# Kernel tuning notes

Hardware: AMD Instinct MI355X
Metric: run time of the kernel (lower is better)

Reference implementation:

```python
import jax, jax.numpy as jnp
import numpy as np

BN_EPS = 1e-5


def _conv1d(x, w, b):
    # x: (B, C, T), w: (O, C, K), torch Conv1d with padding=K//2
    k = w.shape[-1]
    p = k // 2
    out = jax.lax.conv_general_dilated(
        x, w, window_strides=(1,), padding=[(p, p)],
        dimension_numbers=("NCH", "OIH", "NCH"))
    return out + b[None, :, None]


def setup_inputs() -> dict:
    key = jax.random.key(0)
    ks = jax.random.split(key, 16)
    B, C, T, H, NC = 32, 13, 2048, 128, 10
    d = {
        "x": jax.random.normal(ks[0], (B, C, T), jnp.float32),
        "w1": jax.random.normal(ks[1], (H, C, 10), jnp.float32) * 0.1,
        "b1": jax.random.normal(ks[2], (H,), jnp.float32) * 0.1,
        "w2": jax.random.normal(ks[3], (H, C, 20), jnp.float32) * 0.1,
        "b2": jax.random.normal(ks[4], (H,), jnp.float32) * 0.1,
        "w3": jax.random.normal(ks[5], (H, C, 30), jnp.float32) * 0.1,
        "b3": jax.random.normal(ks[6], (H,), jnp.float32) * 0.1,
        "w4": jax.random.normal(ks[7], (H, C, 40), jnp.float32) * 0.1,
        "b4": jax.random.normal(ks[8], (H,), jnp.float32) * 0.1,
        "bn_gamma": jax.random.uniform(ks[9], (4 * H,), jnp.float32, 0.5, 1.5),
        "bn_beta": jax.random.normal(ks[10], (4 * H,), jnp.float32) * 0.1,
        "bn_mean": jnp.zeros((4 * H,), jnp.float32),
        "bn_var": jnp.ones((4 * H,), jnp.float32),
        "logreg_w": jax.random.normal(ks[11], (NC, 4 * H), jnp.float32) * 0.05,
        "logreg_b": jax.random.normal(ks[12], (NC,), jnp.float32) * 0.1,
        "dec_w": jax.random.normal(ks[13], (1, 4 * H), jnp.float32) * 0.05,
        "dec_b": jax.random.normal(ks[14], (1,), jnp.float32) * 0.1,
    }
    return d


def reference(x, w1, b1, w2, b2, w3, b3, w4, b4,
              bn_gamma, bn_beta, bn_mean, bn_var,
              logreg_w, logreg_b, dec_w, dec_b):
    # --- multi-scale shapelet conv + per-prefix cumulative max pooling ---
    feats = []
    for w, b in ((w1, b1), (w2, b2), (w3, b3), (w4, b4)):
        f = _conv1d(x, w, b)                      # (B, H, T+1) (even kernels)
        # original loop: for t in 1..T_out-1 take max over f[:, :, :t]
        # == running (cumulative) max, dropping the last prefix
        cm = jax.lax.cummax(f, axis=2)[:, :, :-1]  # (B, H, T)
        feats.append(jnp.transpose(cm, (0, 2, 1)))  # (B, T, H)
    features = jnp.concatenate(feats, axis=-1)      # (B, T, 4H)

    # --- BatchNorm1d over feature channels (eval mode), dropout = identity ---
    inv = jax.lax.rsqrt(bn_var + BN_EPS)
    features = (features - bn_mean) * (inv * bn_gamma) + bn_beta

    # --- classification head and halting head ---
    logits = jnp.einsum("btf,cf->btc", features, logreg_w) + logreg_b  # (B,T,NC)
    deltas = jnp.einsum("btf,of->bto", features, dec_w) + dec_b        # (B,T,1)
    deltas = jax.nn.softmax(deltas[..., 0], axis=1)                    # (B,T)

    # --- attention budget: pt_t = delta_t * budget_{t-1}; budget decays ---
    B = deltas.shape[0]
    q = 1.0 - deltas                                # (B, T)
    cp = jnp.cumprod(q[:, 1:], axis=1)              # prod_{s=1..t} q_s
    budget = jnp.concatenate([jnp.ones((B, 1), deltas.dtype), cp], axis=1)
    pts_loop = deltas[:, 1:] * budget[:, :-1]       # (B, T-1)
    pts = jnp.concatenate([pts_loop, budget[:, -1:]], axis=1)  # (B, T)

    probs = jax.nn.softmax(logits, axis=-1)  # temperature = 1
    return probs, pts
```

## Files before the change

kernel.cpp:

```cpp
#include <hip/hip_runtime.h>
#include <math.h>

#define NEG_INF (-3.402823466e38f)

typedef float f32x4 __attribute__((ext_vector_type(4)));
typedef short bf16x8 __attribute__((ext_vector_type(8)));

__device__ __forceinline__ unsigned short f2bf(float f) {
    unsigned int u = __float_as_uint(f);
    unsigned int r = (u + 0x7FFFu + ((u >> 16) & 1u)) >> 16;
    return (unsigned short)r;
}
__device__ __forceinline__ float bf2f(unsigned short s) {
    return __uint_as_float(((unsigned int)s) << 16);
}
__device__ __forceinline__ unsigned int pack2(float a, float b) {
    return (unsigned int)f2bf(a) | ((unsigned int)f2bf(b) << 16);
}
__device__ __forceinline__ int swz(int a) { return a ^ (((a >> 5) & 7) << 4); }

__global__ __launch_bounds__(512) void prep_kernel(
    const float* __restrict__ x,
    const float* __restrict__ w1, const float* __restrict__ w2,
    const float* __restrict__ w3, const float* __restrict__ w4,
    const float* __restrict__ bn_gamma, const float* __restrict__ bn_beta,
    const float* __restrict__ bn_mean, const float* __restrict__ bn_var,
    const float* __restrict__ lw, const float* __restrict__ lb,
    const float* __restrict__ dw, const float* __restrict__ db,
    unsigned short* __restrict__ xT, unsigned short* __restrict__ Bfrag,
    unsigned short* __restrict__ hfrag, float* __restrict__ bfo,
    float* __restrict__ dbfo)
{
    int bid = blockIdx.x;
    int tid = threadIdx.x;
    if (bid < 136) {
        int idx = bid * 512 + tid;
        int b = idx / 2176, r = idx - b * 2176;
        int t = r - 20;
        unsigned short row[16];
#pragma unroll
        for (int c = 0; c < 16; ++c) {
            float v = (c < 13 && t >= 0 && t < 2048) ? x[((size_t)(b * 13 + c)) * 2048 + t] : 0.f;
            row[c] = f2bf(v);
        }
        uint4* dst = (uint4*)(xT + (size_t)idx * 16);
        uint4 v0, v1;
        v0.x = row[0] | ((unsigned)row[1] << 16);  v0.y = row[2] | ((unsigned)row[3] << 16);
        v0.z = row[4] | ((unsigned)row[5] << 16);  v0.w = row[6] | ((unsigned)row[7] << 16);
        v1.x = row[8] | ((unsigned)row[9] << 16);  v1.y = row[10] | ((unsigned)row[11] << 16);
        v1.z = row[12] | ((unsigned)row[13] << 16); v1.w = row[14] | ((unsigned)row[15] << 16);
        dst[0] = v0; dst[1] = v1;
    } else if (bid < 186) {
        int idx = (bid - 136) * 512 + tid;
        int lane = idx & 63, frag = idx >> 6;
        int rel, Kc; const float* w;
        if (frag < 40)       { rel = frag;       w = w1; Kc = 10; }
        else if (frag < 120) { rel = frag - 40;  w = w2; Kc = 20; }
        else if (frag < 240) { rel = frag - 120; w = w3; Kc = 30; }
        else                 { rel = frag - 240; w = w4; Kc = 40; }
        int kh = Kc / 2;
        int ht = rel / kh;
        int k0 = rel - ht * kh;
        int h = ht * 16 + (lane & 15);
        int dk = lane >> 5;
        int cbase = 8 * ((lane >> 4) & 1);
        int k = 2 * k0 + dk;
        unsigned short e[8];
#pragma unroll
        for (int j = 0; j < 8; ++j) {
            int c = cbase + j;
            float v = (c < 13) ? w[((size_t)h * 13 + c) * Kc + k] : 0.f;
            e[j] = f2bf(v);
        }
        uint4 pk;
        pk.x = e[0] | ((unsigned)e[1] << 16); pk.y = e[2] | ((unsigned)e[3] << 16);
        pk.z = e[4] | ((unsigned)e[5] << 16); pk.w = e[6] | ((unsigned)e[7] << 16);
        *(uint4*)(Bfrag + (size_t)frag * 512 + lane * 8) = pk;
    } else if (bid == 186) {
        __shared__ float sh[512];
        int j = tid;
        float s = rsqrtf(bn_var[j] + 1e-5f) * bn_gamma[j];
        float shift = bn_beta[j] - bn_mean[j] * s;
        sh[j] = shift;
        __syncthreads();
        if (j < 10) {
            float acc = lb[j];
            for (int q = 0; q < 512; ++q) acc += sh[q] * lw[j * 512 + q];
            bfo[j] = acc;
        } else if (j == 10) {
            float acc = db[0];
            for (int q = 0; q < 512; ++q) acc += sh[q] * dw[q];
            dbfo[0] = acc;
        }
    } else {
        int idx = (bid - 187) * 512 + tid;
        int lane = idx & 63, frag = idx >> 6;
        int n = lane & 15;
        unsigned short e[8];
#pragma unroll
        for (int jj = 0; jj < 8; ++jj) {
            int k = frag * 32 + 8 * (lane >> 4) + jj;
            float s = rsqrtf(bn_var[k] + 1e-5f) * bn_gamma[k];
            float v = (n < 10) ? lw[n * 512 + k] * s : (n == 10) ? dw[k] * s : 0.f;
            e[jj] = f2bf(v);
        }
        uint4 pk;
        pk.x = e[0] | ((unsigned)e[1] << 16); pk.y = e[2] | ((unsigned)e[3] << 16);
        pk.z = e[4] | ((unsigned)e[5] << 16); pk.w = e[6] | ((unsigned)e[7] << 16);
        *(uint4*)(hfrag + (size_t)frag * 512 + lane * 8) = pk;
    }
}

__global__ __launch_bounds__(256, 4) void conv_mfma(
    const unsigned short* __restrict__ xT, const unsigned short* __restrict__ Bfrag,
    const float* __restrict__ b1, const float* __restrict__ b2,
    const float* __restrict__ b3, const float* __restrict__ b4,
    unsigned short* __restrict__ feat, unsigned short* __restrict__ totals)
{
    __shared__ __align__(16) unsigned short lds[2688 + 2 * 64 * 132];
    unsigned short* xs = lds;
    unsigned int* stg32 = (unsigned int*)(lds + 2688);
    const int tid = threadIdx.x;
    const int tq = blockIdx.x & 15;
    const int scale = (blockIdx.x >> 4) & 3;
    const int b = blockIdx.x >> 6;
    const int kh_tab[4] = {5, 10, 15, 20};
    const int so_tab[4] = {0, 40, 120, 240};
    const int KH = kh_tab[scale];
    const int P = 5 * (scale + 1);
    const float* bias = (scale == 0) ? b1 : (scale == 1) ? b2 : (scale == 2) ? b3 : b4;

    const unsigned short* src = xT + ((size_t)b * 2176 + tq * 128) * 16;
#pragma unroll
    for (int it = 0; it < 2; ++it) {
        int c = it * 256 + tid;
        if (c < 336) {
            uint4 v = *(const uint4*)(src + c * 8);
            *(uint4*)((char*)xs + swz(c * 16)) = v;
        }
    }
    __syncthreads();

    const int lane = tid & 63;
    const int wave = tid >> 6;
    const int hgrp = wave & 1;
    const int twq = wave >> 1;
    const int l15 = lane & 15;
    const int g4 = lane >> 4;

    const unsigned short* bfr = Bfrag + ((size_t)(so_tab[scale] + hgrp * 4 * KH)) * 512 + lane * 8;
    float bv[4];
#pragma unroll
    for (int ht = 0; ht < 4; ++ht) bv[ht] = bias[hgrp * 64 + ht * 16 + l15];

    int abase = ((20 - P) + twq * 64 + l15 + (lane >> 5)) * 32 + (g4 & 1) * 16;

    f32x4 acc[4][4];
#pragma unroll
    for (int ht = 0; ht < 4; ++ht)
#pragma unroll
        for (int tt = 0; tt < 4; ++tt)
            acc[ht][tt] = (f32x4){bv[ht], bv[ht], bv[ht], bv[ht]};

#pragma unroll 1
    for (int k0 = 0; k0 < KH; ++k0) {
        bf16x8 B[4], A[4];
#pragma unroll
        for (int ht = 0; ht < 4; ++ht)
            B[ht] = *(const bf16x8*)(bfr + (size_t)(ht * KH + k0) * 512);
#pragma unroll
        for (int tt = 0; tt < 4; ++tt)
            A[tt] = *(const bf16x8*)((const char*)xs + swz(abase + tt * 512 + k0 * 64));
#pragma unroll
        for (int ht = 0; ht < 4; ++ht)
#pragma unroll
            for (int tt = 0; tt < 4; ++tt)
                acc[ht][tt] = __builtin_amdgcn_mfma_f32_16x16x32_bf16(A[tt], B[ht], acc[ht][tt], 0, 0, 0);
    }

    float carry[4] = {NEG_INF, NEG_INF, NEG_INF, NEG_INF};
    const int rq = tq * 2 + twq;
    const int col = hgrp * 64 + l15;

#pragma unroll
    for (int tt = 0; tt < 4; ++tt) {
#pragma unroll
        for (int ht = 0; ht < 4; ++ht) {
            f32x4 v = acc[ht][tt];
            float s0 = v.x;
            float s1 = fmaxf(v.y, s0);
            float s2 = fmaxf(v.z, s1);
            float s3 = fmaxf(v.w, s2);
            float inc = s3;
            float o = __shfl_up(inc, 16); if (lane >= 16) inc = fmaxf(inc, o);
            o = __shfl_up(inc, 32);       if (lane >= 32) inc = fmaxf(inc, o);
            float pre = __shfl_up(inc, 16);
            float base = (lane >= 16) ? fmaxf(carry[ht], pre) : carry[ht];
            s0 = fmaxf(s0, base); s1 = fmaxf(s1, base);
            s2 = fmaxf(s2, base); s3 = fmaxf(s3, base);
            float tot = __shfl(inc, l15 + 48);
            carry[ht] = fmaxf(carry[ht], tot);
            int r2 = twq * 32 + tt * 8 + 2 * g4;
            int cc = col + ht * 16;
            stg32[r2 * 132 + cc]       = pack2(s0, s1);
            stg32[(r2 + 1) * 132 + cc] = pack2(s2, s3);
        }
    }
    if (lane < 16) {
#pragma unroll
        for (int ht = 0; ht < 4; ++ht) {
            int j = scale * 128 + hgrp * 64 + ht * 16 + l15;
            totals[((size_t)b * 32 + rq) * 512 + j] = f2bf(carry[ht]);
        }
    }
    __syncthreads();

    size_t grow = (size_t)b * 2048 + tq * 128;
#pragma unroll
    for (int i = 0; i < 4; ++i) {
        int e = i * 256 + tid;
        int r2 = e >> 4, q = e & 15;
        const unsigned int* p = stg32 + r2 * 132 + q * 8;
        uint4 da = *(const uint4*)(p);
        uint4 db = *(const uint4*)(p + 4);
        uint4 ev, od;
        ev.x = (da.x & 0xffffu) | (da.y << 16);
        ev.y = (da.z & 0xffffu) | (da.w << 16);
        ev.z = (db.x & 0xffffu) | (db.y << 16);
        ev.w = (db.z & 0xffffu) | (db.w << 16);
        od.x = (da.x >> 16) | (da.y & 0xffff0000u);
        od.y = (da.z >> 16) | (da.w & 0xffff0000u);
        od.z = (db.x >> 16) | (db.y & 0xffff0000u);
        od.w = (db.z >> 16) | (db.w & 0xffff0000u);
        size_t base = (grow + 2 * r2) * 512 + scale * 128 + q * 8;
        *(uint4*)(feat + base)       = ev;
        *(uint4*)(feat + base + 512) = od;
    }
}

__global__ __launch_bounds__(256) void head_kernel(
    const unsigned short* __restrict__ feat, const unsigned short* __restrict__ totals,
    const unsigned short* __restrict__ hfrag, const float* __restrict__ bfo,
    const float* __restrict__ dbfo, float* __restrict__ probs,
    float* __restrict__ delta_raw)
{
    __shared__ float pfs[512];
    int b = blockIdx.x >> 5;
    int tc = blockIdx.x & 31;
    int tid = threadIdx.x;
    int lane = tid & 63;
    int wave = tid >> 6;

    for (int j = tid; j < 512; j += 256) {
        float run = NEG_INF;
        for (int qq = 0; qq < tc; ++qq)
            run = fmaxf(run, bf2f(totals[((size_t)b * 32 + qq) * 512 + j]));
        pfs[j] = run;
    }
    __syncthreads();

    bf16x8 Bf[16];
#pragma unroll
    for (int k0 = 0; k0 < 16; ++k0)
        Bf[k0] = *(const bf16x8*)(hfrag + (size_t)k0 * 512 + lane * 8);

    const int n = lane & 15;
    const int g4 = lane >> 4;
    const int tb = tc * 64 + wave * 16;
    const unsigned short* fb = feat + ((size_t)b * 2048 + tb + n) * 512 + 8 * g4;

    float biasv = (n < 10) ? bfo[n] : (n == 10) ? dbfo[0] : 0.f;
    f32x4 acc = (f32x4){biasv, biasv, biasv, biasv};

#pragma unroll
    for (int k0 = 0; k0 < 16; ++k0) {
        bf16x8 a = *(const bf16x8*)(fb + k0 * 32);
        const float* pp = pfs + k0 * 32 + 8 * g4;
        union { unsigned int u[4]; bf16x8 v; } aw;
#pragma unroll
        for (int i = 0; i < 4; ++i) {
            float lo = fmaxf(bf2f((unsigned short)a[2 * i]),     pp[2 * i]);
            float hi = fmaxf(bf2f((unsigned short)a[2 * i + 1]), pp[2 * i + 1]);
            aw.u[i] = (__float_as_uint(lo) >> 16) | (__float_as_uint(hi) & 0xFFFF0000u);
        }
        acc = __builtin_amdgcn_mfma_f32_16x16x32_bf16(aw.v, Bf[k0], acc, 0, 0, 0);
    }

#pragma unroll
    for (int r = 0; r < 4; ++r) {
        float v = acc[r];
        float vm = (n < 10) ? v : NEG_INF;
#pragma unroll
        for (int off = 1; off < 16; off <<= 1)
            vm = fmaxf(vm, __shfl_xor(vm, off, 16));
        float e = (n < 10) ? __expf(v - vm) : 0.f;
        float s = e;
#pragma unroll
        for (int off = 1; off < 16; off <<= 1)
            s += __shfl_xor(s, off, 16);
        int t = tb + g4 * 4 + r;
        if (n < 10) probs[((size_t)b * 2048 + t) * 10 + n] = e / s;
        if (n == 10) delta_raw[b * 2048 + t] = v;
    }
}

__global__ __launch_bounds__(256) void budget_kernel(
    const float* __restrict__ delta_raw, float* __restrict__ pts)
{
    __shared__ float ds[2048];
    __shared__ float red[8];
    int b = blockIdx.x;
    int tid = threadIdx.x;
    int lane = tid & 63, wid = tid >> 6;
    const float* row = delta_raw + b * 2048;
    int base = tid * 8;
    float d[8];
#pragma unroll
    for (int i = 0; i < 8; ++i) d[i] = row[base + i];
    float m = d[0];
#pragma unroll
    for (int i = 1; i < 8; ++i) m = fmaxf(m, d[i]);
#pragma unroll
    for (int off = 1; off < 64; off <<= 1) m = fmaxf(m, __shfl_xor(m, off));
    if (lane == 0) red[wid] = m;
    __syncthreads();
    m = fmaxf(fmaxf(red[0], red[1]), fmaxf(red[2], red[3]));
    float s = 0.f;
#pragma unroll
    for (int i = 0; i < 8; ++i) { d[i] = __expf(d[i] - m); s += d[i]; }
#pragma unroll
    for (int off = 1; off < 64; off <<= 1) s += __shfl_xor(s, off);
    if (lane == 0) red[4 + wid] = s;
    __syncthreads();
    float inv = 1.f / (red[4] + red[5] + red[6] + red[7]);
    float g[8], p = 1.f;
#pragma unroll
    for (int i = 0; i < 8; ++i) {
        d[i] *= inv;
        ds[base + i] = d[i];
        float gv = (base + i == 0) ? 1.f : (1.f - d[i]);
        p *= gv;
        g[i] = p;
    }
    float sp = p;
#pragma unroll
    for (int off = 1; off < 64; off <<= 1) {
        float o = __shfl_up(sp, off);
        if (lane >= off) sp *= o;
    }
    float pre_t = __shfl_up(sp, 1);
    if (lane == 0) pre_t = 1.f;
    if (lane == 63) red[wid] = sp;
    __syncthreads();
    float wpre = 1.f;
#pragma unroll
    for (int w = 0; w < 4; ++w) if (w < wid) wpre *= red[w];
    float pre = wpre * pre_t;
#pragma unroll
    for (int i = 0; i < 8; ++i) {
        int t = base + i;
        float budget = pre * g[i];
        float pt = (t < 2047) ? ds[t + 1] * budget : budget;
        pts[b * 2048 + t] = pt;
    }
}

extern "C" void kernel_launch(void* const* d_in, const int* in_sizes, int n_in,
                              void* d_out, int out_size, void* d_ws, size_t ws_size,
                              hipStream_t stream)
{
    const float* x     = (const float*)d_in[0];
    const float* w1    = (const float*)d_in[1];
    const float* b1    = (const float*)d_in[2];
    const float* w2    = (const float*)d_in[3];
    const float* b2    = (const float*)d_in[4];
    const float* w3    = (const float*)d_in[5];
    const float* b3    = (const float*)d_in[6];
    const float* w4    = (const float*)d_in[7];
    const float* b4    = (const float*)d_in[8];
    const float* gamma = (const float*)d_in[9];
    const float* beta  = (const float*)d_in[10];
    const float* mean  = (const float*)d_in[11];
    const float* var   = (const float*)d_in[12];
    const float* lw    = (const float*)d_in[13];
    const float* lb    = (const float*)d_in[14];
    const float* dw    = (const float*)d_in[15];
    const float* db    = (const float*)d_in[16];

    char* ws = (char*)d_ws;
    unsigned short* feat   = (unsigned short*)ws;
    unsigned short* xT     = (unsigned short*)(ws + 67108864);
    unsigned short* Bfrag  = (unsigned short*)(ws + 69337088);
    unsigned short* totals = (unsigned short*)(ws + 69746688);
    float* draw   = (float*)(ws + 70795264);
    unsigned short* hfrag = (unsigned short*)(ws + 71057408);
    float* bfo    = (float*)(ws + 71073792);
    float* dbfo   = (float*)(ws + 71073856);

    float* probs = (float*)d_out;
    float* pts   = probs + (size_t)32 * 2048 * 10;

    hipLaunchKernelGGL(prep_kernel, dim3(189), dim3(512), 0, stream,
                       x, w1, w2, w3, w4, gamma, beta, mean, var,
                       lw, lb, dw, db, xT, Bfrag, hfrag, bfo, dbfo);
    hipLaunchKernelGGL(conv_mfma, dim3(2048), dim3(256), 0, stream,
                       xT, Bfrag, b1, b2, b3, b4, feat, totals);
    hipLaunchKernelGGL(head_kernel, dim3(1024), dim3(256), 0, stream,
                       feat, totals, hfrag, bfo, dbfo, probs, draw);
    hipLaunchKernelGGL(budget_kernel, dim3(32), dim3(256), 0, stream, draw, pts);
}
```

Baseline: 87.42 us.

## Double-buffer MFMA operand loads and halve conv epilogue staging LDS

The conv kernel's K loop now software-pipelines the global B-fragment and LDS A-fragment loads, fetching the next step's operands while the current MFMAs run. The epilogue keeps the cummax results in the accumulator registers and stages them through a half-size LDS buffer in two passes, one per time-wave group, with nontemporal global stores. The occupancy hint in launch bounds drops from 4 to 2 waves per SIMD to allow more registers for the doubled operand buffers. In exchange it adds an extra barrier and a serialized two-pass epilogue, and occupancy may fall.

```diff
diff --git a/kernel.cpp b/kernel.cpp
--- a/kernel.cpp
+++ b/kernel.cpp
@@ -5,6 +5,7 @@
 
 typedef float f32x4 __attribute__((ext_vector_type(4)));
 typedef short bf16x8 __attribute__((ext_vector_type(8)));
+typedef unsigned int u32x4 __attribute__((ext_vector_type(4)));
 
 __device__ __forceinline__ unsigned short f2bf(float f) {
     unsigned int u = __float_as_uint(f);
@@ -43,8 +44,8 @@
             float v = (c < 13 && t >= 0 && t < 2048) ? x[((size_t)(b * 13 + c)) * 2048 + t] : 0.f;
             row[c] = f2bf(v);
         }
-        uint4* dst = (uint4*)(xT + (size_t)idx * 16);
-        uint4 v0, v1;
+        u32x4* dst = (u32x4*)(xT + (size_t)idx * 16);
+        u32x4 v0, v1;
         v0.x = row[0] | ((unsigned)row[1] << 16);  v0.y = row[2] | ((unsigned)row[3] << 16);
         v0.z = row[4] | ((unsigned)row[5] << 16);  v0.w = row[6] | ((unsigned)row[7] << 16);
         v1.x = row[8] | ((unsigned)row[9] << 16);  v1.y = row[10] | ((unsigned)row[11] << 16);
@@ -72,10 +73,10 @@
             float v = (c < 13) ? w[((size_t)h * 13 + c) * Kc + k] : 0.f;
             e[j] = f2bf(v);
         }
-        uint4 pk;
+        u32x4 pk;
         pk.x = e[0] | ((unsigned)e[1] << 16); pk.y = e[2] | ((unsigned)e[3] << 16);
         pk.z = e[4] | ((unsigned)e[5] << 16); pk.w = e[6] | ((unsigned)e[7] << 16);
-        *(uint4*)(Bfrag + (size_t)frag * 512 + lane * 8) = pk;
+        *(u32x4*)(Bfrag + (size_t)frag * 512 + lane * 8) = pk;
     } else if (bid == 186) {
         __shared__ float sh[512];
         int j = tid;
@@ -104,20 +105,20 @@
             float v = (n < 10) ? lw[n * 512 + k] * s : (n == 10) ? dw[k] * s : 0.f;
             e[jj] = f2bf(v);
         }
-        uint4 pk;
+        u32x4 pk;
         pk.x = e[0] | ((unsigned)e[1] << 16); pk.y = e[2] | ((unsigned)e[3] << 16);
         pk.z = e[4] | ((unsigned)e[5] << 16); pk.w = e[6] | ((unsigned)e[7] << 16);
-        *(uint4*)(hfrag + (size_t)frag * 512 + lane * 8) = pk;
-    }
-}
-
-__global__ __launch_bounds__(256, 4) void conv_mfma(
+        *(u32x4*)(hfrag + (size_t)frag * 512 + lane * 8) = pk;
+    }
+}
+
+__global__ __launch_bounds__(256, 2) void conv_mfma(
     const unsigned short* __restrict__ xT, const unsigned short* __restrict__ Bfrag,
     const float* __restrict__ b1, const float* __restrict__ b2,
     const float* __restrict__ b3, const float* __restrict__ b4,
     unsigned short* __restrict__ feat, unsigned short* __restrict__ totals)
 {
-    __shared__ __align__(16) unsigned short lds[2688 + 2 * 64 * 132];
+    __shared__ __align__(16) unsigned short lds[2688 + 2 * 32 * 132];
     unsigned short* xs = lds;
     unsigned int* stg32 = (unsigned int*)(lds + 2688);
     const int tid = threadIdx.x;
@@ -135,8 +136,8 @@
     for (int it = 0; it < 2; ++it) {
         int c = it * 256 + tid;
         if (c < 336) {
-            uint4 v = *(const uint4*)(src + c * 8);
-            *(uint4*)((char*)xs + swz(c * 16)) = v;
+            u32x4 v = *(const u32x4*)(src + c * 8);
+            *(u32x4*)((char*)xs + swz(c * 16)) = v;
         }
     }
     __syncthreads();
@@ -162,26 +163,35 @@
         for (int tt = 0; tt < 4; ++tt)
             acc[ht][tt] = (f32x4){bv[ht], bv[ht], bv[ht], bv[ht]};
 
+#define LOADB(DST, K) \
+    _Pragma("unroll") for (int ht_ = 0; ht_ < 4; ++ht_) \
+        DST[ht_] = *(const bf16x8*)(bfr + (size_t)(ht_ * KH + (K)) * 512);
+#define LOADA(DST, K) \
+    _Pragma("unroll") for (int tt_ = 0; tt_ < 4; ++tt_) \
+        DST[tt_] = *(const bf16x8*)((const char*)xs + swz(abase + tt_ * 512 + (K) * 64));
+#define MFMA16(AA, BB) \
+    _Pragma("unroll") for (int ht_ = 0; ht_ < 4; ++ht_) \
+        _Pragma("unroll") for (int tt_ = 0; tt_ < 4; ++tt_) \
+            acc[ht_][tt_] = __builtin_amdgcn_mfma_f32_16x16x32_bf16(AA[tt_], BB[ht_], acc[ht_][tt_], 0, 0, 0);
+
+    bf16x8 A0[4], A1[4], B0[4], B1[4];
+    LOADB(B0, 0); LOADA(A0, 0);
+    int k0 = 0;
 #pragma unroll 1
-    for (int k0 = 0; k0 < KH; ++k0) {
-        bf16x8 B[4], A[4];
-#pragma unroll
-        for (int ht = 0; ht < 4; ++ht)
-            B[ht] = *(const bf16x8*)(bfr + (size_t)(ht * KH + k0) * 512);
-#pragma unroll
-        for (int tt = 0; tt < 4; ++tt)
-            A[tt] = *(const bf16x8*)((const char*)xs + swz(abase + tt * 512 + k0 * 64));
-#pragma unroll
-        for (int ht = 0; ht < 4; ++ht)
-#pragma unroll
-            for (int tt = 0; tt < 4; ++tt)
-                acc[ht][tt] = __builtin_amdgcn_mfma_f32_16x16x32_bf16(A[tt], B[ht], acc[ht][tt], 0, 0, 0);
-    }
+    while (k0 + 2 <= KH) {
+        LOADB(B1, k0 + 1); LOADA(A1, k0 + 1);
+        MFMA16(A0, B0);
+        if (k0 + 2 < KH) { LOADB(B0, k0 + 2); LOADA(A0, k0 + 2); }
+        MFMA16(A1, B1);
+        k0 += 2;
+    }
+    if (k0 < KH) { MFMA16(A0, B0); }
+#undef LOADB
+#undef LOADA
+#undef MFMA16
 
     float carry[4] = {NEG_INF, NEG_INF, NEG_INF, NEG_INF};
     const int rq = tq * 2 + twq;
-    const int col = hgrp * 64 + l15;
-
 #pragma unroll
     for (int tt = 0; tt < 4; ++tt) {
 #pragma unroll
@@ -200,10 +210,7 @@
             s2 = fmaxf(s2, base); s3 = fmaxf(s3, base);
             float tot = __shfl(inc, l15 + 48);
             carry[ht] = fmaxf(carry[ht], tot);
-            int r2 = twq * 32 + tt * 8 + 2 * g4;
-            int cc = col + ht * 16;
-            stg32[r2 * 132 + cc]       = pack2(s0, s1);
-            stg32[(r2 + 1) * 132 + cc] = pack2(s2, s3);
+            acc[ht][tt] = (f32x4){s0, s1, s2, s3};
         }
     }
     if (lane < 16) {
@@ -213,28 +220,45 @@
             totals[((size_t)b * 32 + rq) * 512 + j] = f2bf(carry[ht]);
         }
     }
-    __syncthreads();
-
-    size_t grow = (size_t)b * 2048 + tq * 128;
-#pragma unroll
-    for (int i = 0; i < 4; ++i) {
-        int e = i * 256 + tid;
-        int r2 = e >> 4, q = e & 15;
-        const unsigned int* p = stg32 + r2 * 132 + q * 8;
-        uint4 da = *(const uint4*)(p);
-        uint4 db = *(const uint4*)(p + 4);
-        uint4 ev, od;
-        ev.x = (da.x & 0xffffu) | (da.y << 16);
-        ev.y = (da.z & 0xffffu) | (da.w << 16);
-        ev.z = (db.x & 0xffffu) | (db.y << 16);
-        ev.w = (db.z & 0xffffu) | (db.w << 16);
-        od.x = (da.x >> 16) | (da.y & 0xffff0000u);
-        od.y = (da.z >> 16) | (da.w & 0xffff0000u);
-        od.z = (db.x >> 16) | (db.y & 0xffff0000u);
-        od.w = (db.z >> 16) | (db.w & 0xffff0000u);
-        size_t base = (grow + 2 * r2) * 512 + scale * 128 + q * 8;
-        *(uint4*)(feat + base)       = ev;
-        *(uint4*)(feat + base + 512) = od;
+
+#pragma unroll 1
+    for (int half = 0; half < 2; ++half) {
+        if (half) __syncthreads();
+        if (twq == half) {
+#pragma unroll
+            for (int tt = 0; tt < 4; ++tt) {
+#pragma unroll
+                for (int ht = 0; ht < 4; ++ht) {
+                    f32x4 s = acc[ht][tt];
+                    int r2 = tt * 8 + 2 * g4;
+                    int cc = hgrp * 64 + ht * 16 + l15;
+                    stg32[r2 * 132 + cc]       = pack2(s.x, s.y);
+                    stg32[(r2 + 1) * 132 + cc] = pack2(s.z, s.w);
+                }
+            }
+        }
+        __syncthreads();
+        size_t grow = (size_t)b * 2048 + tq * 128 + half * 64;
+#pragma unroll
+        for (int i = 0; i < 2; ++i) {
+            int e = i * 256 + tid;
+            int r2 = e >> 4, q = e & 15;
+            const unsigned int* p = stg32 + r2 * 132 + q * 8;
+            u32x4 da = *(const u32x4*)(p);
+            u32x4 dbb = *(const u32x4*)(p + 4);
+            u32x4 ev, od;
+            ev.x = (da.x & 0xffffu) | (da.y << 16);
+            ev.y = (da.z & 0xffffu) | (da.w << 16);
+            ev.z = (dbb.x & 0xffffu) | (dbb.y << 16);
+            ev.w = (dbb.z & 0xffffu) | (dbb.w << 16);
+            od.x = (da.x >> 16) | (da.y & 0xffff0000u);
+            od.y = (da.z >> 16) | (da.w & 0xffff0000u);
+            od.z = (dbb.x >> 16) | (dbb.y & 0xffff0000u);
+            od.w = (dbb.z >> 16) | (dbb.w & 0xffff0000u);
+            size_t base = (grow + 2 * r2) * 512 + scale * 128 + q * 8;
+            __builtin_nontemporal_store(ev, (u32x4*)(feat + base));
+            __builtin_nontemporal_store(od, (u32x4*)(feat + base + 512));
+        }
     }
 }
 
```

Result: no change. 89.10 us (+1.9%).
